# Kernel tuning notes

Hardware: AMD Instinct MI355X
Metric: run time of the kernel (lower is better)

The kernel has to match this reference:

```python
import jax, jax.numpy as jnp
import numpy as np
from jax import lax

OUT_SCALE = 0.001


def setup_inputs() -> dict:
    key = jax.random.key(0)
    kz, kx = jax.random.split(key)
    z = jax.random.normal(kz, (64, 256, 7, 7), dtype=jnp.float32)
    x = jax.random.normal(kx, (64, 256, 31, 31), dtype=jnp.float32)
    return {"z": z, "x": x}


def reference(z, x):
    # depthwise cross-correlation: each (batch, channel) slice of z is slid
    # over the matching slice of x. Implemented as a grouped conv with
    # feature_group_count = B*C, exactly mirroring torch F.conv2d(groups=B*C).
    B, C, kh, kw = z.shape
    H, W = x.shape[2], x.shape[3]
    x_r = x.reshape(1, B * C, H, W)           # [1, B*C, H, W]
    k_r = z.reshape(B * C, 1, kh, kw)          # [B*C, 1, kh, kw] (OIHW)
    out = lax.conv_general_dilated(
        x_r, k_r,
        window_strides=(1, 1),
        padding="VALID",
        feature_group_count=B * C,
        dimension_numbers=("NCHW", "OIHW", "NCHW"),
    )  # [1, B*C, H-kh+1, W-kw+1]
    out = out.reshape(B, C, out.shape[2], out.shape[3])
    return out * OUT_SCALE
```

## Files before the change

kernel.cpp:

```cpp
#include <hip/hip_runtime.h>


#define KH 7
#define KW 7
#define XH 31
#define XW 31
#define OH 25
#define OW 25
#define NSLICE (64 * 256)
#define SPB 5
#define THREADS 128
#define XS_DW 5120
#define ZS_DW 256
#define OUT_DW (SPB * OH * OW)
#define X_TOTAL_DW (NSLICE * (XH * XW))
#define Z_TOTAL_DW (NSLICE * (KH * KW))

__device__ __forceinline__ void gl_lds16(const float* g, float* l) {
    __builtin_amdgcn_global_load_lds(
        (const __attribute__((address_space(1))) void*)g,
        (__attribute__((address_space(3))) void*)l, 16, 0, 0);
}

__global__ __launch_bounds__(THREADS)
void xcorr_dw_kernel(const float* __restrict__ z,
                     const float* __restrict__ x,
                     float* __restrict__ out) {
    __shared__ float xs[XS_DW];
    __shared__ float zs[ZS_DW];
    const int tid = threadIdx.x;
    const int base_slice = blockIdx.x * SPB;
    const int nsl = min(SPB, NSLICE - base_slice);

    const int g0r  = base_slice * (XH * XW);
    const int pre  = g0r & 3;
    const int g0   = g0r - pre;
    const int zg0r = base_slice * (KH * KW);
    const int prez = zg0r & 3;
    const int zg0  = zg0r - prez;

    #pragma unroll
    for (int k = 0; k < 10; ++k) {
        const int dw  = k * 512 + tid * 4;
        const int gdw = min(g0 + dw, X_TOTAL_DW - 4);
        gl_lds16(x + gdw, xs + dw);
    }
    if (tid < 64) {
        const int gdw = min(zg0 + tid * 4, Z_TOTAL_DW - 4);
        gl_lds16(z + gdw, zs + tid * 4);
    }
    __syncthreads();

    const int sl = tid / 25;
    const int oy = tid - sl * 25;
    const bool active = (sl < nsl);
    float acc[OW] = {};
    if (active) {
        const float* __restrict__ xrow = xs + pre + sl * (XH * XW);
        const float* __restrict__ zrow = zs + prez + sl * (KH * KW);
        #pragma unroll
        for (int i = 0; i < KH; ++i) {
            const float* __restrict__ p = xrow + (oy + i) * XW;
            float f[XW];
            #pragma unroll
            for (int c = 0; c < XW; ++c) f[c] = p[c];
            float w[KW];
            #pragma unroll
            for (int j = 0; j < KW; ++j) w[j] = zrow[i * KW + j];
            #pragma unroll
            for (int j = 0; j < KW; ++j) {
                #pragma unroll
                for (int c = 0; c < OW; ++c)
                    acc[c] = fmaf(f[c + j], w[j], acc[c]);
            }
        }
    }
    __syncthreads();

    if (active) {
        const int fbase = sl * (OH * OW) + oy * OW;
        #pragma unroll
        for (int c = 0; c < OW; ++c) xs[fbase + c] = acc[c] * 0.001f;
    }
    __syncthreads();

    const int n_out = nsl * (OH * OW);
    float* __restrict__ og = out + (size_t)base_slice * (OH * OW);
    for (int d = tid; d < n_out; d += THREADS) og[d] = xs[d];
}

extern "C" void kernel_launch(void* const* d_in, const int* in_sizes, int n_in,
                              void* d_out, int out_size, void* d_ws, size_t ws_size,
                              hipStream_t stream) {
    const float* z = (const float*)d_in[0];
    const float* x = (const float*)d_in[1];
    float* out = (float*)d_out;
    const int nblk = (NSLICE + SPB - 1) / SPB;
    xcorr_dw_kernel<<<dim3(nblk), dim3(THREADS), 0, stream>>>(z, x, out);
}
```

Measured before the change: 112.1 us.

## Make each wave process two slices independently with overlapped load and compute

Each block is split into two waves, and each wave owns two slices in its own LDS region, so all block-wide __syncthreads disappear. Per-wave s_waitcnt vmcnt lets computation on the first slice start while the second slice's x data is still arriving. The filter is now read straight from global memory as wave-uniform values, and each output row is split across two lanes so 50 of 64 lanes are busy. The added launch_bounds hint asks for higher occupancy. In exchange, the code depends on hand-written waitcnt counts and assumes NSLICE divides evenly by the slices per block.

```diff
diff --git a/kernel.cpp b/kernel.cpp
--- a/kernel.cpp
+++ b/kernel.cpp
@@ -8,13 +8,13 @@
 #define OH 25
 #define OW 25
 #define NSLICE (64 * 256)
-#define SPB 5
 #define THREADS 128
-#define XS_DW 5120
-#define ZS_DW 256
-#define OUT_DW (SPB * OH * OW)
-#define X_TOTAL_DW (NSLICE * (XH * XW))
-#define Z_TOTAL_DW (NSLICE * (KH * KW))
+#define SPW 2
+#define SPB (SPW * 2)
+#define XSW_DW 2048
+#define SLICE_X (XH * XW)
+#define SLICE_O (OH * OW)
+#define X_TOTAL_DW (NSLICE * SLICE_X)
 
 __device__ __forceinline__ void gl_lds16(const float* g, float* l) {
     __builtin_amdgcn_global_load_lds(
@@ -22,71 +22,95 @@
         (__attribute__((address_space(3))) void*)l, 16, 0, 0);
 }
 
-__global__ __launch_bounds__(THREADS)
+__global__ __launch_bounds__(THREADS, 4)
 void xcorr_dw_kernel(const float* __restrict__ z,
                      const float* __restrict__ x,
                      float* __restrict__ out) {
-    __shared__ float xs[XS_DW];
-    __shared__ float zs[ZS_DW];
-    const int tid = threadIdx.x;
-    const int base_slice = blockIdx.x * SPB;
-    const int nsl = min(SPB, NSLICE - base_slice);
+    __shared__ float xs[2][XSW_DW];
+    const int tid  = threadIdx.x;
+    const int lane = tid & 63;
+    const int wv   = __builtin_amdgcn_readfirstlane(tid >> 6);
+    float* __restrict__ xsw = xs[wv];
 
-    const int g0r  = base_slice * (XH * XW);
-    const int pre  = g0r & 3;
-    const int g0   = g0r - pre;
-    const int zg0r = base_slice * (KH * KW);
-    const int prez = zg0r & 3;
-    const int zg0  = zg0r - prez;
+    const int wslice = blockIdx.x * SPB + wv * SPW;
+    const int g0r = wslice * SLICE_X;
+    const int pre = g0r & 3;
+    const int g0  = g0r - pre;
 
     #pragma unroll
-    for (int k = 0; k < 10; ++k) {
-        const int dw  = k * 512 + tid * 4;
+    for (int k = 0; k < 8; ++k) {
+        const int dw  = k * 256 + lane * 4;
         const int gdw = min(g0 + dw, X_TOTAL_DW - 4);
-        gl_lds16(x + gdw, xs + dw);
+        gl_lds16(x + gdw, xsw + dw);
     }
-    if (tid < 64) {
-        const int gdw = min(zg0 + tid * 4, Z_TOTAL_DW - 4);
-        gl_lds16(z + gdw, zs + tid * 4);
-    }
-    __syncthreads();
 
-    const int sl = tid / 25;
-    const int oy = tid - sl * 25;
-    const bool active = (sl < nsl);
-    float acc[OW] = {};
-    if (active) {
-        const float* __restrict__ xrow = xs + pre + sl * (XH * XW);
-        const float* __restrict__ zrow = zs + prez + sl * (KH * KW);
+    const float* __restrict__ zw = z + (size_t)wslice * (KH * KW);
+    float* __restrict__ og = out + (size_t)wslice * SLICE_O;
+
+    const int h   = (lane >= OH) ? 1 : 0;
+    const int oy  = h ? (lane - OH) : lane;
+    const bool act = (lane < 2 * OH);
+    const int c0  = h ? 13 : 0;
+
+    asm volatile("s_waitcnt vmcnt(4)" ::: "memory");
+    __builtin_amdgcn_sched_barrier(0);
+    if (act) {
+        float acc[13] = {};
+        const float* __restrict__ xrow = xsw + pre;
         #pragma unroll
         for (int i = 0; i < KH; ++i) {
-            const float* __restrict__ p = xrow + (oy + i) * XW;
-            float f[XW];
+            const float* __restrict__ p = xrow + (oy + i) * XW + c0;
+            float f[19];
             #pragma unroll
-            for (int c = 0; c < XW; ++c) f[c] = p[c];
-            float w[KW];
-            #pragma unroll
-            for (int j = 0; j < KW; ++j) w[j] = zrow[i * KW + j];
+            for (int c = 0; c < 19; ++c) f[c] = p[c];
             #pragma unroll
             for (int j = 0; j < KW; ++j) {
+                const float w = zw[i * KW + j];
                 #pragma unroll
-                for (int c = 0; c < OW; ++c)
-                    acc[c] = fmaf(f[c + j], w[j], acc[c]);
+                for (int c = 0; c < 13; ++c)
+                    acc[c] = fmaf(f[c + j], w, acc[c]);
             }
         }
+        const int fb = oy * OW + c0;
+        #pragma unroll
+        for (int c = 0; c < 12; ++c) xsw[fb + c] = acc[c] * 0.001f;
+        if (!h) xsw[fb + 12] = acc[12] * 0.001f;
     }
-    __syncthreads();
 
-    if (active) {
-        const int fbase = sl * (OH * OW) + oy * OW;
+    asm volatile("s_waitcnt vmcnt(0)" ::: "memory");
+    __builtin_amdgcn_sched_barrier(0);
+    #pragma unroll
+    for (int k = 0; k < 9; ++k) og[k * 64 + lane] = xsw[k * 64 + lane];
+    if (lane < SLICE_O - 576) og[576 + lane] = xsw[576 + lane];
+
+    if (act) {
+        float acc[13] = {};
+        const float* __restrict__ xrow = xsw + pre + SLICE_X;
+        const float* __restrict__ zs = zw + KH * KW;
         #pragma unroll
-        for (int c = 0; c < OW; ++c) xs[fbase + c] = acc[c] * 0.001f;
+        for (int i = 0; i < KH; ++i) {
+            const float* __restrict__ p = xrow + (oy + i) * XW + c0;
+            float f[19];
+            #pragma unroll
+            for (int c = 0; c < 19; ++c) f[c] = p[c];
+            #pragma unroll
+            for (int j = 0; j < KW; ++j) {
+                const float w = zs[i * KW + j];
+                #pragma unroll
+                for (int c = 0; c < 13; ++c)
+                    acc[c] = fmaf(f[c + j], w, acc[c]);
+            }
+        }
+        const int fb = SLICE_O + oy * OW + c0;
+        #pragma unroll
+        for (int c = 0; c < 12; ++c) xsw[fb + c] = acc[c] * 0.001f;
+        if (!h) xsw[fb + 12] = acc[12] * 0.001f;
     }
-    __syncthreads();
-
-    const int n_out = nsl * (OH * OW);
-    float* __restrict__ og = out + (size_t)base_slice * (OH * OW);
-    for (int d = tid; d < n_out; d += THREADS) og[d] = xs[d];
+    #pragma unroll
+    for (int k = 0; k < 9; ++k)
+        og[SLICE_O + k * 64 + lane] = xsw[SLICE_O + k * 64 + lane];
+    if (lane < SLICE_O - 576)
+        og[SLICE_O + 576 + lane] = xsw[SLICE_O + 576 + lane];
 }
 
 extern "C" void kernel_launch(void* const* d_in, const int* in_sizes, int n_in,
@@ -95,6 +119,6 @@
     const float* z = (const float*)d_in[0];
     const float* x = (const float*)d_in[1];
     float* out = (float*)d_out;
-    const int nblk = (NSLICE + SPB - 1) / SPB;
+    const int nblk = NSLICE / SPB;
     xcorr_dw_kernel<<<dim3(nblk), dim3(THREADS), 0, stream>>>(z, x, out);
 }
```

Measured after the change: 113.8 us. No clear change (+1.5%).
